# Optimization experiments

Hardware: AMD Instinct MI355X
Metric: run time of the kernel (lower is better)

## Reference

```python
import jax, jax.numpy as jnp
import numpy as np

N_NODES = 100000
N_EDGES = 1600000
IN_DIM = 128
OUT_DIM = 64
BN_EPS = 1e-5


def setup_inputs() -> dict:
    key = jax.random.key(0)
    ks = jax.random.split(key, 8)
    x = jax.random.normal(ks[0], (N_NODES, IN_DIM), dtype=jnp.float32)
    edge_index = jax.random.randint(ks[1], (2, N_EDGES), 0, N_NODES, dtype=jnp.int64)
    W = jax.random.normal(ks[2], (IN_DIM, OUT_DIM), dtype=jnp.float32) / np.sqrt(IN_DIM)
    b = jax.random.normal(ks[3], (OUT_DIM,), dtype=jnp.float32) * 0.01
    gamma = jax.random.normal(ks[4], (OUT_DIM,), dtype=jnp.float32) * 0.1 + 1.0
    beta = jax.random.normal(ks[5], (OUT_DIM,), dtype=jnp.float32) * 0.1
    run_mean = jax.random.normal(ks[6], (OUT_DIM,), dtype=jnp.float32) * 0.1
    run_var = jax.random.uniform(ks[7], (OUT_DIM,), dtype=jnp.float32, minval=0.5, maxval=1.5)
    return {"x": x, "edge_index": edge_index, "W": W, "b": b,
            "gamma": gamma, "beta": beta, "run_mean": run_mean, "run_var": run_var}


def reference(x, edge_index, W, b, gamma, beta, run_mean, run_var):
    # GCNConv: h = X W; out = D^-1/2 (A + I) D^-1/2 h + b  (add_self_loops=True)
    src = edge_index[0]
    dst = edge_index[1]
    n = x.shape[0]
    # degree from adj_t row-sums (dst counts), +1 for self loop
    deg = jax.ops.segment_sum(jnp.ones_like(dst, dtype=x.dtype), dst, num_segments=n) + 1.0
    d_inv_sqrt = jax.lax.rsqrt(deg)
    norm_e = d_inv_sqrt[src] * d_inv_sqrt[dst]          # [E]
    h = x @ W                                            # [N, OUT_DIM]
    msgs = h[src] * norm_e[:, None]                      # [E, OUT_DIM] gather
    agg = jax.ops.segment_sum(msgs, dst, num_segments=n) # scatter-add
    agg = agg + h * (1.0 / deg)[:, None]                 # self-loop term (d^-1/2 * d^-1/2)
    agg = agg + b                                        # PyG adds bias post-aggregation
    # BatchNorm1d (eval mode: running stats), then ReLU; dropout is identity in eval
    bn = (agg - run_mean) * jax.lax.rsqrt(run_var + BN_EPS) * gamma + beta
    return jax.nn.relu(bn)
```

## Files before the change

### kernel.cpp

```cpp
#include <hip/hip_runtime.h>
#include <hip/hip_bf16.h>

#define IN_DIM 128
#define OUT_DIM 64
#define BN_EPS 1e-5f
#define BSH 7
#define BROWS 128
#define MAXBUCK 800
#define CAP 2560


__global__ __launch_bounds__(1024) void k_bscatter(const int4* __restrict__ src4,
                                                   const int4* __restrict__ dst4, int E4,
                                                   int nbuck, int* __restrict__ gcursor,
                                                   int* __restrict__ recs) {
    __shared__ int hcnt[MAXBUCK];
    __shared__ int hbase[MAXBUCK];
    for (int i = threadIdx.x; i < nbuck; i += 1024) hcnt[i] = 0;
    __syncthreads();

    int i4a = blockIdx.x * 2048 + threadIdx.x;
    int i4b = i4a + 1024;
    bool oka = i4a < E4;
    bool okb = i4b < E4;
    int4 sa, da, sb, db;
    int bk[8], rc[8], rk[8];
    if (oka) {
        sa = src4[i4a]; da = dst4[i4a];
        bk[0] = da.x >> BSH; rc[0] = (sa.x << BSH) | (da.x & (BROWS - 1));
        rk[0] = atomicAdd(&hcnt[bk[0]], 1);
        bk[1] = da.y >> BSH; rc[1] = (sa.y << BSH) | (da.y & (BROWS - 1));
        rk[1] = atomicAdd(&hcnt[bk[1]], 1);
        bk[2] = da.z >> BSH; rc[2] = (sa.z << BSH) | (da.z & (BROWS - 1));
        rk[2] = atomicAdd(&hcnt[bk[2]], 1);
        bk[3] = da.w >> BSH; rc[3] = (sa.w << BSH) | (da.w & (BROWS - 1));
        rk[3] = atomicAdd(&hcnt[bk[3]], 1);
    }
    if (okb) {
        sb = src4[i4b]; db = dst4[i4b];
        bk[4] = db.x >> BSH; rc[4] = (sb.x << BSH) | (db.x & (BROWS - 1));
        rk[4] = atomicAdd(&hcnt[bk[4]], 1);
        bk[5] = db.y >> BSH; rc[5] = (sb.y << BSH) | (db.y & (BROWS - 1));
        rk[5] = atomicAdd(&hcnt[bk[5]], 1);
        bk[6] = db.z >> BSH; rc[6] = (sb.z << BSH) | (db.z & (BROWS - 1));
        rk[6] = atomicAdd(&hcnt[bk[6]], 1);
        bk[7] = db.w >> BSH; rc[7] = (sb.w << BSH) | (db.w & (BROWS - 1));
        rk[7] = atomicAdd(&hcnt[bk[7]], 1);
    }
    __syncthreads();
    for (int i = threadIdx.x; i < nbuck; i += 1024) {
        int c = hcnt[i];
        if (c) hbase[i] = atomicAdd(&gcursor[i], c);
    }
    __syncthreads();
    if (oka) {
        recs[bk[0] * CAP + hbase[bk[0]] + rk[0]] = rc[0];
        recs[bk[1] * CAP + hbase[bk[1]] + rk[1]] = rc[1];
        recs[bk[2] * CAP + hbase[bk[2]] + rk[2]] = rc[2];
        recs[bk[3] * CAP + hbase[bk[3]] + rk[3]] = rc[3];
    }
    if (okb) {
        recs[bk[4] * CAP + hbase[bk[4]] + rk[4]] = rc[4];
        recs[bk[5] * CAP + hbase[bk[5]] + rk[5]] = rc[5];
        recs[bk[6] * CAP + hbase[bk[6]] + rk[6]] = rc[6];
        recs[bk[7] * CAP + hbase[bk[7]] + rk[7]] = rc[7];
    }
}

__global__ __launch_bounds__(1024) void k_sort(const int* __restrict__ gcnt,
                                               const int* __restrict__ recs,
                                               int* __restrict__ sorted,
                                               int* __restrict__ offs,
                                               int* __restrict__ deg,
                                               float* __restrict__ dinv, int N) {
    __shared__ int hist[BROWS];
    __shared__ int cur[BROWS];
    __shared__ int sh[BROWS];
    int b = blockIdx.x;
    int cnt = gcnt[b];
    int e0 = b * CAP, e1 = e0 + cnt;
    int tid = threadIdx.x;
    if (tid < BROWS) hist[tid] = 0;
    __syncthreads();
    for (int e = e0 + tid; e < e1; e += 1024)
        atomicAdd(&hist[recs[e] & (BROWS - 1)], 1);
    __syncthreads();
    int v = (tid < BROWS) ? hist[tid] : 0;
    if (tid < BROWS) sh[tid] = v;
    __syncthreads();
    for (int d = 1; d < BROWS; d <<= 1) {
        int t = (tid < BROWS && tid >= d) ? sh[tid - d] : 0;
        __syncthreads();
        if (tid < BROWS) sh[tid] += t;
        __syncthreads();
    }
    if (tid < BROWS) {
        int pre = sh[tid] - v;
        cur[tid] = pre;
        int n = (b << BSH) + tid;
        if (n < N) {
            offs[n] = e0 + pre;
            deg[n] = v;
            dinv[n] = rsqrtf((float)(v + 1));
        }
    }
    __syncthreads();
    for (int e = e0 + tid; e < e1; e += 1024) {
        int r = recs[e];
        int p = atomicAdd(&cur[r & (BROWS - 1)], 1);
        sorted[e0 + p] = r >> BSH;
    }
}

__global__ __launch_bounds__(256) void k_gemm(const float* __restrict__ x,
                                              const float* __restrict__ W,
                                              const float* __restrict__ dinv,
                                              __hip_bfloat16* __restrict__ mbf, int N) {
    __shared__ unsigned Wp[(IN_DIM / 2) * OUT_DIM];
    __shared__ float xl[16 * IN_DIM];

    for (int i = threadIdx.x; i < (IN_DIM / 2) * OUT_DIM; i += 256) {
        int k2 = i >> 6, ln = i & 63;
        float w0 = W[(2 * k2) * OUT_DIM + ln];
        float w1 = W[(2 * k2 + 1) * OUT_DIM + ln];
        unsigned u0 = (unsigned)__bfloat16_as_ushort(__float2bfloat16(w0));
        unsigned u1 = (unsigned)__bfloat16_as_ushort(__float2bfloat16(w1));
        Wp[i] = (u1 << 16) | u0;
    }

    int node0 = blockIdx.x * 16;
    for (int i = threadIdx.x; i < 16 * IN_DIM / 4; i += 256) {
        int n = node0 + (i >> 5);
        if (n < N)
            ((float4*)xl)[i] = ((const float4*)x)[(size_t)node0 * (IN_DIM / 4) + i];
    }
    __syncthreads();

    int wave = threadIdx.x >> 6;
    int lane = threadIdx.x & 63;
    int nb = node0 + wave * 4;

    float acc[4] = {0.f, 0.f, 0.f, 0.f};
    for (int k0 = 0; k0 < IN_DIM; k0 += 4) {
        unsigned wa = Wp[(k0 >> 1) * OUT_DIM + lane];
        unsigned wb = Wp[((k0 >> 1) + 1) * OUT_DIM + lane];
        float w0 = __uint_as_float(wa << 16);
        float w1 = __uint_as_float(wa & 0xffff0000u);
        float w2 = __uint_as_float(wb << 16);
        float w3 = __uint_as_float(wb & 0xffff0000u);
        float4 xv0 = ((float4*)xl)[((wave * 4 + 0) * IN_DIM + k0) >> 2];
        float4 xv1 = ((float4*)xl)[((wave * 4 + 1) * IN_DIM + k0) >> 2];
        float4 xv2 = ((float4*)xl)[((wave * 4 + 2) * IN_DIM + k0) >> 2];
        float4 xv3 = ((float4*)xl)[((wave * 4 + 3) * IN_DIM + k0) >> 2];
        acc[0] += xv0.x * w0 + xv0.y * w1 + xv0.z * w2 + xv0.w * w3;
        acc[1] += xv1.x * w0 + xv1.y * w1 + xv1.z * w2 + xv1.w * w3;
        acc[2] += xv2.x * w0 + xv2.y * w1 + xv2.z * w2 + xv2.w * w3;
        acc[3] += xv3.x * w0 + xv3.y * w1 + xv3.z * w2 + xv3.w * w3;
    }
    #pragma unroll
    for (int j = 0; j < 4; ++j) {
        int n = nb + j;
        if (n < N)
            mbf[(size_t)n * OUT_DIM + lane] = __float2bfloat16(acc[j] * dinv[n]);
    }
}

__device__ inline void accum_bf8(float* acc, uint4 r) {
    const unsigned* u = (const unsigned*)&r;
    #pragma unroll
    for (int i = 0; i < 4; ++i) {
        acc[2 * i]     += __uint_as_float(u[i] << 16);
        acc[2 * i + 1] += __uint_as_float(u[i] & 0xffff0000u);
    }
}

__global__ __launch_bounds__(256) void k_agg(const int* __restrict__ offs,
                                             const int* __restrict__ deg,
                                             const int* __restrict__ sorted,
                                             const float* __restrict__ dinv,
                                             const uint4* __restrict__ mbf4,
                                             const float* __restrict__ b,
                                             const float* __restrict__ gamma,
                                             const float* __restrict__ beta,
                                             const float* __restrict__ mean,
                                             const float* __restrict__ var,
                                             float* __restrict__ out, int N) {
    int wid = (blockIdx.x * 256 + threadIdx.x) >> 6;
    int lane = threadIdx.x & 63;
    if (wid >= N) return;
    int n = wid;
    int s0 = offs[n];
    int s1 = s0 + deg[n];
    int g = lane >> 3;
    int sub = lane & 7;

    float acc[8] = {0.f, 0.f, 0.f, 0.f, 0.f, 0.f, 0.f, 0.f};
    int e = s0;
    for (; e + 16 <= s1; e += 16) {
        int sA = sorted[e + g];
        int sB = sorted[e + 8 + g];
        uint4 ra = mbf4[(size_t)sA * 8 + sub];
        uint4 rb = mbf4[(size_t)sB * 8 + sub];
        accum_bf8(acc, ra);
        accum_bf8(acc, rb);
    }
    for (; e < s1; e += 8) {
        int idx = e + g;
        if (idx < s1) {
            uint4 ra = mbf4[(size_t)sorted[idx] * 8 + sub];
            accum_bf8(acc, ra);
        }
    }

    #pragma unroll
    for (int mask = 8; mask <= 32; mask <<= 1) {
        #pragma unroll
        for (int k = 0; k < 8; ++k)
            acc[k] += __shfl_xor(acc[k], mask, 64);
    }

    if (lane < 8) {
        uint4 sf = mbf4[(size_t)n * 8 + lane];
        float s[8];
        {
            const unsigned* u = (const unsigned*)&sf;
            #pragma unroll
            for (int i = 0; i < 4; ++i) {
                s[2 * i]     = __uint_as_float(u[i] << 16);
                s[2 * i + 1] = __uint_as_float(u[i] & 0xffff0000u);
            }
        }
        float dn = dinv[n];
        float4 gg0 = ((const float4*)gamma)[lane * 2], gg1 = ((const float4*)gamma)[lane * 2 + 1];
        float4 vv0 = ((const float4*)var)[lane * 2],   vv1 = ((const float4*)var)[lane * 2 + 1];
        float4 bb0 = ((const float4*)b)[lane * 2],     bb1 = ((const float4*)b)[lane * 2 + 1];
        float4 mm0 = ((const float4*)mean)[lane * 2],  mm1 = ((const float4*)mean)[lane * 2 + 1];
        float4 ee0 = ((const float4*)beta)[lane * 2],  ee1 = ((const float4*)beta)[lane * 2 + 1];
        float gv[8] = {gg0.x, gg0.y, gg0.z, gg0.w, gg1.x, gg1.y, gg1.z, gg1.w};
        float vv[8] = {vv0.x, vv0.y, vv0.z, vv0.w, vv1.x, vv1.y, vv1.z, vv1.w};
        float bv[8] = {bb0.x, bb0.y, bb0.z, bb0.w, bb1.x, bb1.y, bb1.z, bb1.w};
        float mv[8] = {mm0.x, mm0.y, mm0.z, mm0.w, mm1.x, mm1.y, mm1.z, mm1.w};
        float ev[8] = {ee0.x, ee0.y, ee0.z, ee0.w, ee1.x, ee1.y, ee1.z, ee1.w};
        float o[8];
        #pragma unroll
        for (int k = 0; k < 8; ++k) {
            float sc = gv[k] * rsqrtf(vv[k] + BN_EPS);
            float vval = ((acc[k] + s[k]) * dn + bv[k] - mv[k]) * sc + ev[k];
            o[k] = vval > 0.f ? vval : 0.f;
        }
        float4* op = (float4*)&out[(size_t)n * OUT_DIM + lane * 8];
        op[0] = make_float4(o[0], o[1], o[2], o[3]);
        op[1] = make_float4(o[4], o[5], o[6], o[7]);
    }
}


extern "C" void kernel_launch(void* const* d_in, const int* in_sizes, int n_in,
                              void* d_out, int out_size, void* d_ws, size_t ws_size,
                              hipStream_t stream) {
    const float* x     = (const float*)d_in[0];
    const int*   edges = (const int*)d_in[1];
    const float* W     = (const float*)d_in[2];
    const float* b     = (const float*)d_in[3];
    const float* gamma = (const float*)d_in[4];
    const float* beta  = (const float*)d_in[5];
    const float* rmean = (const float*)d_in[6];
    const float* rvar  = (const float*)d_in[7];
    float* out = (float*)d_out;

    int N = in_sizes[0] / IN_DIM;
    int E = in_sizes[1] / 2;
    const int* src = edges;
    const int* dst = edges + E;

    int nbuck = (N + BROWS - 1) >> BSH;
    int E4 = E >> 2;
    int nebk = (E4 + 2047) / 2048;

    char* ws = (char*)d_ws;
    size_t mB = ((size_t)N * OUT_DIM * sizeof(__hip_bfloat16) + 255) & ~(size_t)255;
    size_t pB = ((size_t)nbuck * CAP * sizeof(int) + 255) & ~(size_t)255;
    __hip_bfloat16* mbf = (__hip_bfloat16*)(ws);
    int*   recs    = (int*)  (ws + mB);
    int*   sorted  = (int*)  (ws + mB + pB);
    int*   gcursor = (int*)  (ws + mB + 2 * pB);
    int*   offs    = gcursor + nbuck;
    int*   deg     = offs + N;
    float* dinv    = (float*)(deg + N);

    hipMemsetAsync(gcursor, 0, (size_t)nbuck * sizeof(int), stream);

    k_bscatter<<<nebk, 1024, 0, stream>>>((const int4*)src, (const int4*)dst, E4,
                                          nbuck, gcursor, recs);
    k_sort<<<nbuck, 1024, 0, stream>>>(gcursor, recs, sorted, offs, deg, dinv, N);
    k_gemm<<<(N + 15) / 16, 256, 0, stream>>>(x, W, dinv, mbf, N);
    k_agg<<<(N + 3) / 4, 256, 0, stream>>>(offs, deg, sorted, dinv, (const uint4*)mbf,
                                           b, gamma, beta, rmean, rvar, out, N);
}
```

Baseline: 244.7 us.

## Use MFMA bf16 instructions for the X·W GEMM with prepacked weight fragments

```diff
diff --git a/kernel.cpp b/kernel.cpp
--- a/kernel.cpp
+++ b/kernel.cpp
@@ -8,6 +8,9 @@
 #define BROWS 128
 #define MAXBUCK 800
 #define CAP 2560
+
+typedef __attribute__((ext_vector_type(8))) short short8v;
+typedef __attribute__((ext_vector_type(4))) float f32x4;
 
 
 __global__ __launch_bounds__(1024) void k_bscatter(const int4* __restrict__ src4,
@@ -112,61 +115,86 @@
     }
 }
 
+__global__ __launch_bounds__(256) void k_packW(const float* __restrict__ W,
+                                               unsigned short* __restrict__ WF) {
+    for (int i = threadIdx.x; i < 16 * 64 * 8; i += 256) {
+        int tile = i >> 9, rest = i & 511, l = rest >> 3, j = rest & 7;
+        int kt = tile >> 2, nt = tile & 3;
+        int k = kt * 32 + (l >> 4) * 8 + j;
+        int d = nt * 16 + (l & 15);
+        WF[i] = __bfloat16_as_ushort(__float2bfloat16(W[k * OUT_DIM + d]));
+    }
+}
+
 __global__ __launch_bounds__(256) void k_gemm(const float* __restrict__ x,
-                                              const float* __restrict__ W,
+                                              const unsigned short* __restrict__ WF,
                                               const float* __restrict__ dinv,
                                               __hip_bfloat16* __restrict__ mbf, int N) {
-    __shared__ unsigned Wp[(IN_DIM / 2) * OUT_DIM];
-    __shared__ float xl[16 * IN_DIM];
-
-    for (int i = threadIdx.x; i < (IN_DIM / 2) * OUT_DIM; i += 256) {
-        int k2 = i >> 6, ln = i & 63;
-        float w0 = W[(2 * k2) * OUT_DIM + ln];
-        float w1 = W[(2 * k2 + 1) * OUT_DIM + ln];
-        unsigned u0 = (unsigned)__bfloat16_as_ushort(__float2bfloat16(w0));
-        unsigned u1 = (unsigned)__bfloat16_as_ushort(__float2bfloat16(w1));
-        Wp[i] = (u1 << 16) | u0;
-    }
-
-    int node0 = blockIdx.x * 16;
-    for (int i = threadIdx.x; i < 16 * IN_DIM / 4; i += 256) {
-        int n = node0 + (i >> 5);
-        if (n < N)
-            ((float4*)xl)[i] = ((const float4*)x)[(size_t)node0 * (IN_DIM / 4) + i];
-    }
-    __syncthreads();
-
+    __shared__ unsigned short WFl[16 * 64 * 8];
+    __shared__ unsigned short XL[64 * IN_DIM];
+
+    for (int i = threadIdx.x; i < 1024; i += 256)
+        ((uint4*)WFl)[i] = ((const uint4*)WF)[i];
+
+    int node0 = blockIdx.x * 64;
+    for (int i = threadIdx.x; i < 2048; i += 256) {
+        int row = i >> 5;
+        int c8  = (i & 31) * 8;
+        int gn = node0 + row;
+        float4 v = (gn < N) ? ((const float4*)x)[(size_t)gn * 32 + (i & 31)]
+                            : make_float4(0.f, 0.f, 0.f, 0.f);
+        unsigned u0 = ((unsigned)__bfloat16_as_ushort(__float2bfloat16(v.y)) << 16)
+                    |  (unsigned)__bfloat16_as_ushort(__float2bfloat16(v.x));
+        unsigned u1 = ((unsigned)__bfloat16_as_ushort(__float2bfloat16(v.w)) << 16)
+                    |  (unsigned)__bfloat16_as_ushort(__float2bfloat16(v.z));
+        int byte = row * 256 + (c8 ^ ((row & 7) << 4));
+        *(uint2*)((char*)XL + byte) = make_uint2(u0, u1);
+    }
+    __syncthreads();
+
+    int lane = threadIdx.x & 63;
     int wave = threadIdx.x >> 6;
-    int lane = threadIdx.x & 63;
-    int nb = node0 + wave * 4;
-
-    float acc[4] = {0.f, 0.f, 0.f, 0.f};
-    for (int k0 = 0; k0 < IN_DIM; k0 += 4) {
-        unsigned wa = Wp[(k0 >> 1) * OUT_DIM + lane];
-        unsigned wb = Wp[((k0 >> 1) + 1) * OUT_DIM + lane];
-        float w0 = __uint_as_float(wa << 16);
-        float w1 = __uint_as_float(wa & 0xffff0000u);
-        float w2 = __uint_as_float(wb << 16);
-        float w3 = __uint_as_float(wb & 0xffff0000u);
-        float4 xv0 = ((float4*)xl)[((wave * 4 + 0) * IN_DIM + k0) >> 2];
-        float4 xv1 = ((float4*)xl)[((wave * 4 + 1) * IN_DIM + k0) >> 2];
-        float4 xv2 = ((float4*)xl)[((wave * 4 + 2) * IN_DIM + k0) >> 2];
-        float4 xv3 = ((float4*)xl)[((wave * 4 + 3) * IN_DIM + k0) >> 2];
-        acc[0] += xv0.x * w0 + xv0.y * w1 + xv0.z * w2 + xv0.w * w3;
-        acc[1] += xv1.x * w0 + xv1.y * w1 + xv1.z * w2 + xv1.w * w3;
-        acc[2] += xv2.x * w0 + xv2.y * w1 + xv2.z * w2 + xv2.w * w3;
-        acc[3] += xv3.x * w0 + xv3.y * w1 + xv3.z * w2 + xv3.w * w3;
-    }
-    #pragma unroll
-    for (int j = 0; j < 4; ++j) {
-        int n = nb + j;
-        if (n < N)
-            mbf[(size_t)n * OUT_DIM + lane] = __float2bfloat16(acc[j] * dinv[n]);
-    }
-}
-
-__device__ inline void accum_bf8(float* acc, uint4 r) {
-    const unsigned* u = (const unsigned*)&r;
+    int ra = lane & 15;
+    int kg = lane >> 4;
+    int r = wave * 16 + ra;
+
+    short8v a[4];
+    #pragma unroll
+    for (int kt = 0; kt < 4; ++kt) {
+        int byte = r * 256 + (((kt * 64) + kg * 16) ^ ((r & 7) << 4));
+        a[kt] = *(const short8v*)((const char*)XL + byte);
+    }
+
+    f32x4 acc[4];
+    #pragma unroll
+    for (int nt = 0; nt < 4; ++nt) acc[nt] = (f32x4){0.f, 0.f, 0.f, 0.f};
+
+    #pragma unroll
+    for (int nt = 0; nt < 4; ++nt) {
+        #pragma unroll
+        for (int kt = 0; kt < 4; ++kt) {
+            short8v bfr = *(const short8v*)&WFl[((kt * 4 + nt) * 64 + lane) * 8];
+            acc[nt] = __builtin_amdgcn_mfma_f32_16x16x32_bf16(a[kt], bfr, acc[nt], 0, 0, 0);
+        }
+    }
+
+    int nb = node0 + wave * 16;
+    #pragma unroll
+    for (int rr = 0; rr < 4; ++rr) {
+        int node = nb + kg * 4 + rr;
+        if (node < N) {
+            float dn = dinv[node];
+            #pragma unroll
+            for (int nt = 0; nt < 4; ++nt) {
+                mbf[(size_t)node * OUT_DIM + nt * 16 + ra] =
+                    __float2bfloat16(acc[nt][rr] * dn);
+            }
+        }
+    }
+}
+
+__device__ inline void accum_bf8(float* acc, uint4 rr) {
+    const unsigned* u = (const unsigned*)&rr;
     #pragma unroll
     for (int i = 0; i < 4; ++i) {
         acc[2 * i]     += __uint_as_float(u[i] << 16);
@@ -287,13 +315,15 @@
     int*   offs    = gcursor + nbuck;
     int*   deg     = offs + N;
     float* dinv    = (float*)(deg + N);
+    unsigned short* wfg = (unsigned short*)(dinv + N);
 
     hipMemsetAsync(gcursor, 0, (size_t)nbuck * sizeof(int), stream);
 
+    k_packW<<<1, 256, 0, stream>>>(W, wfg);
     k_bscatter<<<nebk, 1024, 0, stream>>>((const int4*)src, (const int4*)dst, E4,
                                           nbuck, gcursor, recs);
     k_sort<<<nbuck, 1024, 0, stream>>>(gcursor, recs, sorted, offs, deg, dinv, N);
-    k_gemm<<<(N + 15) / 16, 256, 0, stream>>>(x, W, dinv, mbf, N);
+    k_gemm<<<(N + 63) / 64, 256, 0, stream>>>(x, wfg, dinv, mbf, N);
     k_agg<<<(N + 3) / 4, 256, 0, stream>>>(offs, deg, sorted, dinv, (const uint4*)mbf,
                                            b, gamma, beta, rmean, rvar, out, N);
 }
```

Result: faster. 211.1 us (-13.7%).
